# Kernel tuning notes

Measured on AMD Instinct MI355X. Metric: run time of the kernel, lower is better.

## Reference

```python
import jax, jax.numpy as jnp
import numpy as np

B, N, D, E, H, C = 262144, 5, 20, 16, 32, 4  # batch, nodes, node_dim, emo_emb, hidden, n_emotions
LN_EPS = 1e-5


def setup_inputs() -> dict:
    key = jax.random.key(0)
    ks = jax.random.split(key, 16)
    s = 0.1
    return {
        "neutral_feat": jax.random.normal(ks[0], (B, N, D), jnp.float32),
        "emo_idx": jax.random.randint(ks[1], (B,), 0, C, jnp.int64),
        "emo_emb": jax.random.normal(ks[2], (C, E), jnp.float32) * s,
        "A_w1": jax.random.normal(ks[3], (E, 32), jnp.float32) * s,
        "A_b1": jnp.zeros((32,), jnp.float32),
        "A_w2": jax.random.normal(ks[4], (32, N * N), jnp.float32) * s,
        "A_b2": jnp.zeros((N * N,), jnp.float32),
        "enc_w": jax.random.normal(ks[5], (D + E, H), jnp.float32) * s,
        "enc_b": jnp.zeros((H,), jnp.float32),
        "ln_g": jnp.ones((H,), jnp.float32),
        "ln_b": jnp.zeros((H,), jnp.float32),
        "out_w1": jax.random.normal(ks[6], (H, H), jnp.float32) * s,
        "out_b1": jnp.zeros((H,), jnp.float32),
        "out_w2": jax.random.normal(ks[7], (H, D), jnp.float32) * s,
        "out_b2": jnp.zeros((D,), jnp.float32),
        "cls_w": jax.random.normal(ks[8], (H * N, C), jnp.float32) * s,
        "cls_b": jnp.zeros((C,), jnp.float32),
    }


def _layernorm(x, g, b):
    mu = jnp.mean(x, axis=-1, keepdims=True)
    var = jnp.var(x, axis=-1, keepdims=True)
    return (x - mu) * jax.lax.rsqrt(var + LN_EPS) * g + b


def reference(neutral_feat, emo_idx, emo_emb, A_w1, A_b1, A_w2, A_b2,
              enc_w, enc_b, ln_g, ln_b, out_w1, out_b1, out_w2, out_b2,
              cls_w, cls_b):
    b = neutral_feat.shape[0]
    e = emo_emb[emo_idx]                                        # (B, E)
    # emotion-specific adjacency: MLP -> (B, N*N) -> row softmax
    a = jax.nn.relu(e @ A_w1 + A_b1) @ A_w2 + A_b2
    A = jax.nn.softmax(a.reshape(b, N, N), axis=-1)             # (B, N, N)
    # node encoder on [neutral_feat ; e]
    e_exp = jnp.broadcast_to(e[:, None, :], (b, N, E))
    x = jnp.concatenate([neutral_feat, e_exp], axis=-1)         # (B, N, D+E)
    h = jax.nn.relu(_layernorm(x @ enc_w + enc_b, ln_g, ln_b))  # (B, N, H)
    h_agg = jnp.einsum('bij,bjh->bih', A, h)                    # (B, N, H)
    delta = jax.nn.relu(h_agg @ out_w1 + out_b1) @ out_w2 + out_b2  # (B, N, D)
    aux_logits = h_agg.reshape(b, N * H) @ cls_w + cls_b        # (B, C)
    return (delta, aux_logits, A)
```

## Files before the change

### kernel.cpp

```cpp
#include <hip/hip_runtime.h>
#include <math.h>

#define B_TOT   262144ll
#define LOG_OFF 26214400ll
#define A_OFF   27262976ll

#define WS_A4   0
#define WS_ENCB 112

#define L_A4   0
#define L_ENCB 104
#define L_CLS  232
#define L_HST  872
#define L_AUX  9512
#define L_TOT  10472

__device__ __forceinline__ void fma4(float a, const float4& w, float* acc) {
    acc[0] = fmaf(a, w.x, acc[0]);
    acc[1] = fmaf(a, w.y, acc[1]);
    acc[2] = fmaf(a, w.z, acc[2]);
    acc[3] = fmaf(a, w.w, acc[3]);
}

__global__ void __launch_bounds__(128) precomp_kernel(
    const float* __restrict__ emo_emb, const float* __restrict__ A_w1,
    const float* __restrict__ A_b1, const float* __restrict__ A_w2,
    const float* __restrict__ A_b2, const float* __restrict__ enc_w,
    const float* __restrict__ enc_b, float* __restrict__ wsf)
{
    __shared__ float hid[4][32];
    __shared__ float av[4][25];
    const int t = threadIdx.x;
    const int c = t >> 5, m = t & 31;

    float acc = A_b1[m];
    #pragma unroll
    for (int k = 0; k < 16; ++k)
        acc = fmaf(emo_emb[c*16 + k], A_w1[k*32 + m], acc);
    hid[c][m] = fmaxf(acc, 0.f);
    __syncthreads();

    if (m < 25) {
        float a2 = A_b2[m];
        #pragma unroll
        for (int k = 0; k < 32; ++k)
            a2 = fmaf(hid[c][k], A_w2[k*25 + m], a2);
        av[c][m] = a2;
    }
    __syncthreads();

    if (m < 5) {
        float v[5];
        #pragma unroll
        for (int q = 0; q < 5; ++q) v[q] = av[c][m*5 + q];
        float mx = v[0];
        #pragma unroll
        for (int q = 1; q < 5; ++q) mx = fmaxf(mx, v[q]);
        float ssum = 0.f;
        #pragma unroll
        for (int q = 0; q < 5; ++q) { v[q] = expf(v[q] - mx); ssum += v[q]; }
        float inv = 1.f / ssum;
        #pragma unroll
        for (int q = 0; q < 5; ++q) wsf[WS_A4 + c*25 + m*5 + q] = v[q] * inv;
    }

    float eb = enc_b[m];
    #pragma unroll
    for (int k = 0; k < 16; ++k)
        eb = fmaf(emo_emb[c*16 + k], enc_w[(20 + k)*32 + m], eb);
    wsf[WS_ENCB + c*32 + m] = eb;
}

__global__ void __launch_bounds__(256) main_kernel(
    const float* __restrict__ nf, const int* __restrict__ emo_idx,
    const float* __restrict__ enc_w, const float* __restrict__ ln_g,
    const float* __restrict__ ln_b, const float* __restrict__ w1,
    const float* __restrict__ b1, const float* __restrict__ w2,
    const float* __restrict__ b2, const float* __restrict__ clsw,
    const float* __restrict__ clsb, const float* __restrict__ wsf,
    float* __restrict__ out)
{
    __shared__ __align__(16) float s[L_TOT];
    const int tid = threadIdx.x;

    for (int t = tid; t < 640; t += 256) s[L_CLS + t] = clsw[t];
    if (tid < 128) s[L_ENCB + tid] = wsf[WS_ENCB + tid];
    if (tid < 100) s[L_A4 + tid]   = wsf[WS_A4 + tid];
    __syncthreads();

    const int wave = tid >> 6, lane = tid & 63;
    const int g = lane / 5, n = lane - g*5;
    const long long b = (long long)blockIdx.x * 48 + wave*12 + g;
    const bool act = (lane < 60) && (b < B_TOT);

    const float4* encw4 = (const float4*)enc_w;
    const float4* w1_4  = (const float4*)w1;
    const float4* w2_4  = (const float4*)w2;
    const float4* b1_4  = (const float4*)b1;
    const float4* lg4   = (const float4*)ln_g;
    const float4* lb4   = (const float4*)ln_b;
    const float4* b2_4  = (const float4*)b2;

    int emo = 0;
    float x[20];
    #pragma unroll
    for (int d = 0; d < 20; ++d) x[d] = 0.f;
    if (act) {
        emo = emo_idx[b];
        const float4* xp = (const float4*)(nf + b*100ll + n*20);
        #pragma unroll
        for (int t = 0; t < 5; ++t) {
            float4 v = xp[t];
            x[4*t+0] = v.x; x[4*t+1] = v.y; x[4*t+2] = v.z; x[4*t+3] = v.w;
        }
    }

    float y[32];
    {
        const float4* ev = (const float4*)&s[L_ENCB];
        #pragma unroll
        for (int j4 = 0; j4 < 8; ++j4) {
            float4 v = ev[emo*8 + j4];
            y[4*j4+0] = v.x; y[4*j4+1] = v.y; y[4*j4+2] = v.z; y[4*j4+3] = v.w;
        }
        #pragma unroll
        for (int d = 0; d < 20; ++d) {
            float xv = x[d];
            #pragma unroll
            for (int j4 = 0; j4 < 8; ++j4)
                fma4(xv, encw4[d*8 + j4], y + 4*j4);
        }
    }

    {
        float sum = 0.f;
        #pragma unroll
        for (int j = 0; j < 32; ++j) sum += y[j];
        float mu = sum * 0.03125f;
        float sq = 0.f;
        #pragma unroll
        for (int j = 0; j < 32; ++j) { float d = y[j] - mu; sq = fmaf(d, d, sq); }
        float rs = rsqrtf(fmaf(sq, 0.03125f, 1e-5f));
        #pragma unroll
        for (int j4 = 0; j4 < 8; ++j4) {
            float4 gg = lg4[j4], bb = lb4[j4];
            float h0 = fmaf((y[4*j4+0] - mu) * rs, gg.x, bb.x);
            float h1 = fmaf((y[4*j4+1] - mu) * rs, gg.y, bb.y);
            float h2 = fmaf((y[4*j4+2] - mu) * rs, gg.z, bb.z);
            float h3 = fmaf((y[4*j4+3] - mu) * rs, gg.w, bb.w);
            y[4*j4+0] = fmaxf(h0, 0.f); y[4*j4+1] = fmaxf(h1, 0.f);
            y[4*j4+2] = fmaxf(h2, 0.f); y[4*j4+3] = fmaxf(h3, 0.f);
        }
    }

    if (act) {
        float4* hp = (float4*)&s[L_HST + (wave*60 + lane)*36];
        #pragma unroll
        for (int t = 0; t < 8; ++t)
            hp[t] = make_float4(y[4*t], y[4*t+1], y[4*t+2], y[4*t+3]);
    }
    asm volatile("s_waitcnt lgkmcnt(0)" ::: "memory");

    float hagg[32];
    #pragma unroll
    for (int j = 0; j < 32; ++j) hagg[j] = 0.f;
    if (act) {
        #pragma unroll
        for (int nn = 0; nn < 5; ++nn) {
            float a = s[L_A4 + emo*25 + n*5 + nn];
            const float4* rp = (const float4*)&s[L_HST + (wave*60 + g*5 + nn)*36];
            #pragma unroll
            for (int t = 0; t < 8; ++t)
                fma4(a, rp[t], hagg + 4*t);
        }
    }

    float r[32];
    {
        #pragma unroll
        for (int j4 = 0; j4 < 8; ++j4) {
            float4 v = b1_4[j4];
            r[4*j4+0] = v.x; r[4*j4+1] = v.y; r[4*j4+2] = v.z; r[4*j4+3] = v.w;
        }
        #pragma unroll
        for (int k = 0; k < 32; ++k) {
            float hv = hagg[k];
            #pragma unroll
            for (int j4 = 0; j4 < 8; ++j4)
                fma4(hv, w1_4[k*8 + j4], r + 4*j4);
        }
        #pragma unroll
        for (int j = 0; j < 32; ++j) r[j] = fmaxf(r[j], 0.f);
    }

    float dl[20];
    {
        #pragma unroll
        for (int d4 = 0; d4 < 5; ++d4) {
            float4 v = b2_4[d4];
            dl[4*d4+0] = v.x; dl[4*d4+1] = v.y; dl[4*d4+2] = v.z; dl[4*d4+3] = v.w;
        }
        #pragma unroll
        for (int k = 0; k < 32; ++k) {
            float rv = r[k];
            #pragma unroll
            for (int d4 = 0; d4 < 5; ++d4)
                fma4(rv, w2_4[k*5 + d4], dl + 4*d4);
        }
    }
    if (act) {
        float4* op = (float4*)(out + b*100ll + n*20);
        #pragma unroll
        for (int t = 0; t < 5; ++t)
            op[t] = make_float4(dl[4*t], dl[4*t+1], dl[4*t+2], dl[4*t+3]);
    }

    float4 p = make_float4(0.f, 0.f, 0.f, 0.f);
    {
        const float4* cv = (const float4*)&s[L_CLS];
        #pragma unroll
        for (int j = 0; j < 32; ++j) {
            float hv = hagg[j];
            float4 w = cv[n*32 + j];
            p.x = fmaf(hv, w.x, p.x); p.y = fmaf(hv, w.y, p.y);
            p.z = fmaf(hv, w.z, p.z); p.w = fmaf(hv, w.w, p.w);
        }
    }
    float4 cb = *(const float4*)clsb;
    if (act) {
        *(float4*)&s[L_AUX + ((wave*12 + g)*5 + n)*4] = p;
        #pragma unroll
        for (int q = 0; q < 5; ++q)
            out[A_OFF + b*25ll + n*5 + q] = s[L_A4 + emo*25 + n*5 + q];
    }
    asm volatile("s_waitcnt lgkmcnt(0)" ::: "memory");
    if (act && n == 0) {
        float4 acc = cb;
        #pragma unroll
        for (int nn = 0; nn < 5; ++nn) {
            float4 pv = *(const float4*)&s[L_AUX + ((wave*12 + g)*5 + nn)*4];
            acc.x += pv.x; acc.y += pv.y; acc.z += pv.z; acc.w += pv.w;
        }
        *(float4*)(out + LOG_OFF + b*4ll) = acc;
    }
}

extern "C" void kernel_launch(void* const* d_in, const int* in_sizes, int n_in,
                              void* d_out, int out_size, void* d_ws, size_t ws_size,
                              hipStream_t stream) {
    const float* nf      = (const float*)d_in[0];
    const int*   emo_idx = (const int*)  d_in[1];
    const float* emo_emb = (const float*)d_in[2];
    const float* A_w1    = (const float*)d_in[3];
    const float* A_b1    = (const float*)d_in[4];
    const float* A_w2    = (const float*)d_in[5];
    const float* A_b2    = (const float*)d_in[6];
    const float* enc_w   = (const float*)d_in[7];
    const float* enc_b   = (const float*)d_in[8];
    const float* ln_g    = (const float*)d_in[9];
    const float* ln_b    = (const float*)d_in[10];
    const float* out_w1  = (const float*)d_in[11];
    const float* out_b1  = (const float*)d_in[12];
    const float* out_w2  = (const float*)d_in[13];
    const float* out_b2  = (const float*)d_in[14];
    const float* cls_w   = (const float*)d_in[15];
    const float* cls_b   = (const float*)d_in[16];
    float* wsf = (float*)d_ws;
    float* outf = (float*)d_out;

    precomp_kernel<<<1, 128, 0, stream>>>(emo_emb, A_w1, A_b1, A_w2, A_b2,
                                          enc_w, enc_b, wsf);
    const int grid = (262144 + 47) / 48;
    main_kernel<<<grid, 256, 0, stream>>>(nf, emo_idx, enc_w, ln_g, ln_b,
                                          out_w1, out_b1, out_w2, out_b2,
                                          cls_w, cls_b, wsf, outf);
}
```

Before: 358.8 us.

## Map one batch element per thread, keep node states in registers

Changes the work split so each thread handles a whole batch sample (all 5 nodes) instead of one node per lane. Node hidden states stay in registers, so the LDS staging, the cross-lane aggregation and the logits reduction through shared memory go away. Classifier and bias weights are now read from global or constant memory rather than LDS, and the launch bound asks for 2 blocks per CU. The cost is a much larger register footprint (h[5][32] plus temporaries), which may cause spills. Global loads and stores per thread also become strided by 400 bytes across lanes, which hurts coalescing.

```diff
diff --git a/kernel.cpp b/kernel.cpp
--- a/kernel.cpp
+++ b/kernel.cpp
@@ -7,13 +7,6 @@
 
 #define WS_A4   0
 #define WS_ENCB 112
-
-#define L_A4   0
-#define L_ENCB 104
-#define L_CLS  232
-#define L_HST  872
-#define L_AUX  9512
-#define L_TOT  10472
 
 __device__ __forceinline__ void fma4(float a, const float4& w, float* acc) {
     acc[0] = fmaf(a, w.x, acc[0]);
@@ -71,7 +64,7 @@
     wsf[WS_ENCB + c*32 + m] = eb;
 }
 
-__global__ void __launch_bounds__(256) main_kernel(
+__global__ void __launch_bounds__(256, 2) main_kernel(
     const float* __restrict__ nf, const int* __restrict__ emo_idx,
     const float* __restrict__ enc_w, const float* __restrict__ ln_g,
     const float* __restrict__ ln_b, const float* __restrict__ w1,
@@ -80,18 +73,13 @@
     const float* __restrict__ clsb, const float* __restrict__ wsf,
     float* __restrict__ out)
 {
-    __shared__ __align__(16) float s[L_TOT];
+    __shared__ float sA4[100];
     const int tid = threadIdx.x;
-
-    for (int t = tid; t < 640; t += 256) s[L_CLS + t] = clsw[t];
-    if (tid < 128) s[L_ENCB + tid] = wsf[WS_ENCB + tid];
-    if (tid < 100) s[L_A4 + tid]   = wsf[WS_A4 + tid];
+    if (tid < 100) sA4[tid] = wsf[WS_A4 + tid];
     __syncthreads();
 
-    const int wave = tid >> 6, lane = tid & 63;
-    const int g = lane / 5, n = lane - g*5;
-    const long long b = (long long)blockIdx.x * 48 + wave*12 + g;
-    const bool act = (lane < 60) && (b < B_TOT);
+    const long long b = (long long)blockIdx.x * 256 + tid;
+    const int emo = emo_idx[b];
 
     const float4* encw4 = (const float4*)enc_w;
     const float4* w1_4  = (const float4*)w1;
@@ -100,29 +88,32 @@
     const float4* lg4   = (const float4*)ln_g;
     const float4* lb4   = (const float4*)ln_b;
     const float4* b2_4  = (const float4*)b2;
-
-    int emo = 0;
-    float x[20];
+    const float4* cw4   = (const float4*)clsw;
+    const float4  cb    = *(const float4*)clsb;
+
+    float eb[32];
+    {
+        const float4* ebp = (const float4*)(wsf + WS_ENCB + emo*32);
+        #pragma unroll
+        for (int j4 = 0; j4 < 8; ++j4) {
+            float4 v = ebp[j4];
+            eb[4*j4+0]=v.x; eb[4*j4+1]=v.y; eb[4*j4+2]=v.z; eb[4*j4+3]=v.w;
+        }
+    }
+
+    float h[5][32];
+    const float4* xbase = (const float4*)(nf + b*100ll);
     #pragma unroll
-    for (int d = 0; d < 20; ++d) x[d] = 0.f;
-    if (act) {
-        emo = emo_idx[b];
-        const float4* xp = (const float4*)(nf + b*100ll + n*20);
+    for (int n = 0; n < 5; ++n) {
+        float x[20];
         #pragma unroll
         for (int t = 0; t < 5; ++t) {
-            float4 v = xp[t];
-            x[4*t+0] = v.x; x[4*t+1] = v.y; x[4*t+2] = v.z; x[4*t+3] = v.w;
-        }
-    }
-
-    float y[32];
-    {
-        const float4* ev = (const float4*)&s[L_ENCB];
-        #pragma unroll
-        for (int j4 = 0; j4 < 8; ++j4) {
-            float4 v = ev[emo*8 + j4];
-            y[4*j4+0] = v.x; y[4*j4+1] = v.y; y[4*j4+2] = v.z; y[4*j4+3] = v.w;
-        }
+            float4 v = xbase[n*5 + t];
+            x[4*t+0]=v.x; x[4*t+1]=v.y; x[4*t+2]=v.z; x[4*t+3]=v.w;
+        }
+        float y[32];
+        #pragma unroll
+        for (int j = 0; j < 32; ++j) y[j] = eb[j];
         #pragma unroll
         for (int d = 0; d < 20; ++d) {
             float xv = x[d];
@@ -130,9 +121,6 @@
             for (int j4 = 0; j4 < 8; ++j4)
                 fma4(xv, encw4[d*8 + j4], y + 4*j4);
         }
-    }
-
-    {
         float sum = 0.f;
         #pragma unroll
         for (int j = 0; j < 32; ++j) sum += y[j];
@@ -144,43 +132,48 @@
         #pragma unroll
         for (int j4 = 0; j4 < 8; ++j4) {
             float4 gg = lg4[j4], bb = lb4[j4];
-            float h0 = fmaf((y[4*j4+0] - mu) * rs, gg.x, bb.x);
-            float h1 = fmaf((y[4*j4+1] - mu) * rs, gg.y, bb.y);
-            float h2 = fmaf((y[4*j4+2] - mu) * rs, gg.z, bb.z);
-            float h3 = fmaf((y[4*j4+3] - mu) * rs, gg.w, bb.w);
-            y[4*j4+0] = fmaxf(h0, 0.f); y[4*j4+1] = fmaxf(h1, 0.f);
-            y[4*j4+2] = fmaxf(h2, 0.f); y[4*j4+3] = fmaxf(h3, 0.f);
-        }
-    }
-
-    if (act) {
-        float4* hp = (float4*)&s[L_HST + (wave*60 + lane)*36];
-        #pragma unroll
-        for (int t = 0; t < 8; ++t)
-            hp[t] = make_float4(y[4*t], y[4*t+1], y[4*t+2], y[4*t+3]);
-    }
-    asm volatile("s_waitcnt lgkmcnt(0)" ::: "memory");
-
-    float hagg[32];
-    #pragma unroll
-    for (int j = 0; j < 32; ++j) hagg[j] = 0.f;
-    if (act) {
-        #pragma unroll
-        for (int nn = 0; nn < 5; ++nn) {
-            float a = s[L_A4 + emo*25 + n*5 + nn];
-            const float4* rp = (const float4*)&s[L_HST + (wave*60 + g*5 + nn)*36];
-            #pragma unroll
-            for (int t = 0; t < 8; ++t)
-                fma4(a, rp[t], hagg + 4*t);
-        }
-    }
-
-    float r[32];
-    {
+            h[n][4*j4+0] = fmaxf(fmaf((y[4*j4+0]-mu)*rs, gg.x, bb.x), 0.f);
+            h[n][4*j4+1] = fmaxf(fmaf((y[4*j4+1]-mu)*rs, gg.y, bb.y), 0.f);
+            h[n][4*j4+2] = fmaxf(fmaf((y[4*j4+2]-mu)*rs, gg.z, bb.z), 0.f);
+            h[n][4*j4+3] = fmaxf(fmaf((y[4*j4+3]-mu)*rs, gg.w, bb.w), 0.f);
+        }
+    }
+
+    float logits[4] = {cb.x, cb.y, cb.z, cb.w};
+    for (int i = 0; i < 5; ++i) {
+        float ai[5];
+        #pragma unroll
+        for (int nn = 0; nn < 5; ++nn) ai[nn] = sA4[emo*25 + i*5 + nn];
+        #pragma unroll
+        for (int nn = 0; nn < 5; ++nn)
+            out[A_OFF + b*25ll + i*5 + nn] = ai[nn];
+
+        float hagg[32];
+        #pragma unroll
+        for (int j = 0; j < 32; ++j) {
+            float v = ai[0] * h[0][j];
+            v = fmaf(ai[1], h[1][j], v);
+            v = fmaf(ai[2], h[2][j], v);
+            v = fmaf(ai[3], h[3][j], v);
+            v = fmaf(ai[4], h[4][j], v);
+            hagg[j] = v;
+        }
+
+        #pragma unroll
+        for (int j = 0; j < 32; ++j) {
+            float hv = hagg[j];
+            float4 w = cw4[i*32 + j];
+            logits[0] = fmaf(hv, w.x, logits[0]);
+            logits[1] = fmaf(hv, w.y, logits[1]);
+            logits[2] = fmaf(hv, w.z, logits[2]);
+            logits[3] = fmaf(hv, w.w, logits[3]);
+        }
+
+        float r[32];
         #pragma unroll
         for (int j4 = 0; j4 < 8; ++j4) {
             float4 v = b1_4[j4];
-            r[4*j4+0] = v.x; r[4*j4+1] = v.y; r[4*j4+2] = v.z; r[4*j4+3] = v.w;
+            r[4*j4+0]=v.x; r[4*j4+1]=v.y; r[4*j4+2]=v.z; r[4*j4+3]=v.w;
         }
         #pragma unroll
         for (int k = 0; k < 32; ++k) {
@@ -191,58 +184,26 @@
         }
         #pragma unroll
         for (int j = 0; j < 32; ++j) r[j] = fmaxf(r[j], 0.f);
-    }
-
-    float dl[20];
-    {
+
+        float* orow = out + b*100ll + i*20;
         #pragma unroll
         for (int d4 = 0; d4 < 5; ++d4) {
-            float4 v = b2_4[d4];
-            dl[4*d4+0] = v.x; dl[4*d4+1] = v.y; dl[4*d4+2] = v.z; dl[4*d4+3] = v.w;
-        }
-        #pragma unroll
-        for (int k = 0; k < 32; ++k) {
-            float rv = r[k];
+            float4 acc = b2_4[d4];
             #pragma unroll
-            for (int d4 = 0; d4 < 5; ++d4)
-                fma4(rv, w2_4[k*5 + d4], dl + 4*d4);
-        }
-    }
-    if (act) {
-        float4* op = (float4*)(out + b*100ll + n*20);
-        #pragma unroll
-        for (int t = 0; t < 5; ++t)
-            op[t] = make_float4(dl[4*t], dl[4*t+1], dl[4*t+2], dl[4*t+3]);
-    }
-
-    float4 p = make_float4(0.f, 0.f, 0.f, 0.f);
-    {
-        const float4* cv = (const float4*)&s[L_CLS];
-        #pragma unroll
-        for (int j = 0; j < 32; ++j) {
-            float hv = hagg[j];
-            float4 w = cv[n*32 + j];
-            p.x = fmaf(hv, w.x, p.x); p.y = fmaf(hv, w.y, p.y);
-            p.z = fmaf(hv, w.z, p.z); p.w = fmaf(hv, w.w, p.w);
-        }
-    }
-    float4 cb = *(const float4*)clsb;
-    if (act) {
-        *(float4*)&s[L_AUX + ((wave*12 + g)*5 + n)*4] = p;
-        #pragma unroll
-        for (int q = 0; q < 5; ++q)
-            out[A_OFF + b*25ll + n*5 + q] = s[L_A4 + emo*25 + n*5 + q];
-    }
-    asm volatile("s_waitcnt lgkmcnt(0)" ::: "memory");
-    if (act && n == 0) {
-        float4 acc = cb;
-        #pragma unroll
-        for (int nn = 0; nn < 5; ++nn) {
-            float4 pv = *(const float4*)&s[L_AUX + ((wave*12 + g)*5 + nn)*4];
-            acc.x += pv.x; acc.y += pv.y; acc.z += pv.z; acc.w += pv.w;
-        }
-        *(float4*)(out + LOG_OFF + b*4ll) = acc;
-    }
+            for (int k = 0; k < 32; ++k) {
+                float rv = r[k];
+                float4 w = w2_4[k*5 + d4];
+                acc.x = fmaf(rv, w.x, acc.x);
+                acc.y = fmaf(rv, w.y, acc.y);
+                acc.z = fmaf(rv, w.z, acc.z);
+                acc.w = fmaf(rv, w.w, acc.w);
+            }
+            *(float4*)(orow + 4*d4) = acc;
+        }
+    }
+
+    *(float4*)(out + LOG_OFF + b*4ll) =
+        make_float4(logits[0], logits[1], logits[2], logits[3]);
 }
 
 extern "C" void kernel_launch(void* const* d_in, const int* in_sizes, int n_in,
@@ -270,8 +231,7 @@
 
     precomp_kernel<<<1, 128, 0, stream>>>(emo_emb, A_w1, A_b1, A_w2, A_b2,
                                           enc_w, enc_b, wsf);
-    const int grid = (262144 + 47) / 48;
-    main_kernel<<<grid, 256, 0, stream>>>(nf, emo_idx, enc_w, ln_g, ln_b,
+    main_kernel<<<1024, 256, 0, stream>>>(nf, emo_idx, enc_w, ln_g, ln_b,
                                           out_w1, out_b1, out_w2, out_b2,
                                           cls_w, cls_b, wsf, outf);
 }
```

New measurement: 573.8 us. +59.9%, slower.
